# Performance work log

Measured on AMD Instinct MI355X. Metric: run time of the kernel, lower is better.

Reference implementation:

```python
import jax, jax.numpy as jnp
import numpy as np

N_NODES = 20000
N_EDGES = 320000
N_GRAPHS = 256
F_IN = 128
HID = 512


def _xavier(key, shape, gain=1.0):
    fan_out, fan_in = shape
    a = gain * np.sqrt(6.0 / (fan_in + fan_out))
    return jax.random.uniform(key, shape, jnp.float32, -a, a)


def setup_inputs() -> dict:
    key = jax.random.key(0)
    ks = jax.random.split(key, 9)
    x = jax.random.normal(ks[0], (N_NODES, F_IN), jnp.float32)
    edge_index = jax.random.randint(ks[1], (2, N_EDGES), 0, N_NODES, dtype=jnp.int64)
    batch = jnp.sort(jax.random.randint(ks[2], (N_NODES,), 0, N_GRAPHS, dtype=jnp.int64))
    return {
        "x": x,
        "edge_index": edge_index,
        "batch": batch,
        "lin_W": _xavier(ks[3], (HID, F_IN)),
        "lin_b": jnp.zeros((HID,), jnp.float32),
        "W1": _xavier(ks[4], (HID, F_IN)),
        "b1": jnp.zeros((HID,), jnp.float32),
        "W2": _xavier(ks[5], (HID, HID)),
        "b2": jnp.zeros((HID,), jnp.float32),
        "W3": _xavier(ks[6], (HID, HID)),
        "b3": jnp.zeros((HID,), jnp.float32),
        "W4": _xavier(ks[7], (HID, HID)),
        "b4": jnp.zeros((HID,), jnp.float32),
    }


def _gcn_conv(x, W, b, src, dst, norm, n_nodes):
    # PyG GCNConv: h = x @ W.T; out_i = sum_j norm_ij * h_j (scatter over dst) + b
    h = x @ W.T
    msg = h[src] * norm[:, None]  # [E', H] gather + scale
    return jax.ops.segment_sum(msg, dst, num_segments=n_nodes) + b


def reference(x, edge_index, batch, lin_W, lin_b, W1, b1, W2, b2, W3, b3, W4, b4):
    n = x.shape[0]
    loop = jnp.arange(n, dtype=edge_index.dtype)
    src = jnp.concatenate([edge_index[0], loop])
    dst = jnp.concatenate([edge_index[1], loop])
    # symmetric normalization D^-1/2 (A+I) D^-1/2, degree = in-degree over dst
    deg = jax.ops.segment_sum(jnp.ones_like(src, dtype=x.dtype), dst, num_segments=n)
    dis = jnp.where(deg > 0, jax.lax.rsqrt(deg), 0.0)
    norm = dis[src] * dis[dst]

    x_l = x @ lin_W.T + lin_b  # dead code when act=None (kept for faithfulness)

    h1 = _gcn_conv(x, W1, b1, src, dst, norm, n)
    h2 = _gcn_conv(h1, W2, b2, src, dst, norm, n)
    h3 = _gcn_conv(h2, W3, b3, src, dst, norm, n)
    h4 = _gcn_conv(h3, W4, b4, src, dst, norm, n)
    h = jnp.concatenate([h1, h2, h3, h4], axis=1)  # [N, 4*HID]

    h_pooled = jax.ops.segment_max(h, batch, num_segments=N_GRAPHS)
    h_pos = (h > 0).astype(h.dtype)
    counts = jax.ops.segment_sum(jnp.ones((n,), h.dtype), batch, num_segments=N_GRAPHS)
    h_pos_pooled = jax.ops.segment_sum(h_pos, batch, num_segments=N_GRAPHS) / jnp.maximum(counts, 1.0)[:, None]
    return jnp.concatenate([h_pooled, h_pos_pooled], axis=1)  # [G, 8*HID]
```

## Files before the change

### kernel.cpp

```cpp
#include <hip/hip_runtime.h>
#include <cfloat>
#include <cmath>

#define F_IN 128
#define HID 512

typedef short bf16x8 __attribute__((ext_vector_type(8)));
typedef float f32x4 __attribute__((ext_vector_type(4)));

__device__ static inline void split_bf16(float v, short& hi, short& lo) {
    unsigned u = __float_as_uint(v);
    unsigned r = u + 0x7FFF + ((u >> 16) & 1);
    hi = (short)(r >> 16);
    float hf = __uint_as_float(((unsigned)(unsigned short)hi) << 16);
    float res = v - hf;
    unsigned u2 = __float_as_uint(res);
    unsigned r2 = u2 + 0x7FFF + ((u2 >> 16) & 1);
    lo = (short)(r2 >> 16);
}

__device__ static inline void gload_lds16(const void* g, void* l) {
    __builtin_amdgcn_global_load_lds(
        (const __attribute__((address_space(1))) unsigned int*)g,
        (__attribute__((address_space(3))) unsigned int*)l,
        16, 0, 0);
}


__global__ void zero_kernel(int* __restrict__ a, int n) {
    int i = blockIdx.x * blockDim.x + threadIdx.x;
    if (i < n) a[i] = 0;
}

__global__ void count_in_kernel(const int* __restrict__ dst, int* __restrict__ cnt, int E) {
    int e = blockIdx.x * blockDim.x + threadIdx.x;
    if (e < E) atomicAdd(&cnt[dst[e]], 1);
}

__global__ void scan_kernel(const int* __restrict__ cnt, int* __restrict__ offs, int n) {
    __shared__ int buf[1024];
    __shared__ int carry_s;
    if (threadIdx.x == 0) carry_s = 0;
    __syncthreads();
    for (int base = 0; base < n; base += 1024) {
        int i = base + threadIdx.x;
        int v = (i < n) ? cnt[i] : 0;
        buf[threadIdx.x] = v;
        __syncthreads();
        for (int s = 1; s < 1024; s <<= 1) {
            int t = (threadIdx.x >= s) ? buf[threadIdx.x - s] : 0;
            __syncthreads();
            buf[threadIdx.x] += t;
            __syncthreads();
        }
        int total = buf[1023];
        if (i < n) offs[i] = carry_s + buf[threadIdx.x] - v;
        __syncthreads();
        if (threadIdx.x == 0) carry_s += total;
        __syncthreads();
    }
    if (threadIdx.x == 0) offs[n] = carry_s;
}

__global__ void dis_kernel(const int* __restrict__ offs, float* __restrict__ dis, int n) {
    int i = blockIdx.x * blockDim.x + threadIdx.x;
    if (i < n) dis[i] = rsqrtf((float)(offs[i + 1] - offs[i] + 1));
}

__global__ void fill_csr_kernel(const int* __restrict__ src, const int* __restrict__ dst,
                                const int* __restrict__ offs, int* __restrict__ cnt,
                                unsigned short* __restrict__ csr, int E) {
    int e = blockIdx.x * blockDim.x + threadIdx.x;
    if (e < E) {
        int d = dst[e];
        int p = atomicSub(&cnt[d], 1);
        csr[offs[d] + p - 1] = (unsigned short)src[e];
    }
}

__global__ void starts_kernel(const int* __restrict__ batch, int* __restrict__ starts,
                              int n, int G) {
    int i = blockIdx.x * blockDim.x + threadIdx.x;
    if (i >= n) return;
    int b = batch[i];
    if (i == 0) {
        for (int g = 0; g <= b; g++) starts[g] = 0;
    } else {
        int bp = batch[i - 1];
        for (int g = bp + 1; g <= b; g++) starts[g] = i;
    }
    if (i == n - 1) {
        for (int g = b + 1; g <= G; g++) starts[g] = n;
    }
}

__global__ void wconv_kernel(const float* __restrict__ W1, const float* __restrict__ W2,
                             const float* __restrict__ W3, const float* __restrict__ W4,
                             short* __restrict__ Whi, short* __restrict__ Wlo) {
    int i = blockIdx.x * blockDim.x + threadIdx.x;
    const int n1 = HID * F_IN, nk = HID * HID;
    float v;
    if (i < n1) v = W1[i];
    else if (i < n1 + nk) v = W2[i - n1];
    else if (i < n1 + 2 * nk) v = W3[i - n1 - nk];
    else if (i < n1 + 3 * nk) v = W4[i - n1 - 2 * nk];
    else return;
    short h, l;
    split_bf16(v, h, l);
    Whi[i] = h;
    Wlo[i] = l;
}

template <int F, int CHUNKS>
__global__ __launch_bounds__(64) void agg_chunk_kernel(
    const float* __restrict__ H, const float* __restrict__ dis,
    const int* __restrict__ offs, const unsigned short* __restrict__ csr,
    short* __restrict__ Ahi, short* __restrict__ Alo, int n) {
    int blk = blockIdx.x;
    int i = blk / CHUNKS;
    int chunk = blk % CHUNKS;
    int col = chunk * 64 + threadIdx.x;
    const float* Hc = H + col;

    float di = dis[i];
    float a = di * Hc[(size_t)i * F];
    int e = offs[i], e1 = offs[i + 1];
    for (; e + 8 <= e1; e += 8) {
        int j0 = csr[e],     j1 = csr[e + 1], j2 = csr[e + 2], j3 = csr[e + 3];
        int j4 = csr[e + 4], j5 = csr[e + 5], j6 = csr[e + 6], j7 = csr[e + 7];
        float d0 = dis[j0], d1 = dis[j1], d2 = dis[j2], d3 = dis[j3];
        float d4 = dis[j4], d5 = dis[j5], d6 = dis[j6], d7 = dis[j7];
        float r0 = Hc[(size_t)j0 * F], r1 = Hc[(size_t)j1 * F];
        float r2 = Hc[(size_t)j2 * F], r3 = Hc[(size_t)j3 * F];
        float r4 = Hc[(size_t)j4 * F], r5 = Hc[(size_t)j5 * F];
        float r6 = Hc[(size_t)j6 * F], r7 = Hc[(size_t)j7 * F];
        a += d0 * r0 + d1 * r1 + d2 * r2 + d3 * r3;
        a += d4 * r4 + d5 * r5 + d6 * r6 + d7 * r7;
    }
    for (; e < e1; e++) {
        int j = csr[e];
        a += dis[j] * Hc[(size_t)j * F];
    }
    a *= di;
    short h, l;
    split_bf16(a, h, l);
    Ahi[(size_t)i * F + col] = h;
    Alo[(size_t)i * F + col] = l;
}

__global__ __launch_bounds__(256) void gemm_mfma_kernel(
    const short* __restrict__ Ahi, const short* __restrict__ Alo,
    const short* __restrict__ Whi, const short* __restrict__ Wlo,
    const float* __restrict__ bias, float* __restrict__ C,
    int M, int K, int Nout) {
    __shared__ __attribute__((aligned(16))) short lds[4][4096];

    int tid = threadIdx.x;
    int w = tid >> 6, l = tid & 63;
    int m0 = blockIdx.x * 128, n0 = blockIdx.y * 128;
    int lrow = l & 15, lq = l >> 4;

    const short* gp = (w == 0) ? Ahi : (w == 1) ? Alo : (w == 2) ? Whi : Wlo;
    int base_mn = (w < 2) ? m0 : n0;

    f32x4 acc[4][4];
    #pragma unroll
    for (int i = 0; i < 4; i++)
        #pragma unroll
        for (int j = 0; j < 4; j++) acc[i][j] = (f32x4){0.f, 0.f, 0.f, 0.f};

    int wm = w >> 1, wn = w & 1;

    for (int k0 = 0; k0 < K; k0 += 32) {
        const short* gbase = gp + (size_t)(base_mn + lrow) * K + (k0 + lq * 8);
        #pragma unroll
        for (int s = 0; s < 8; s++) {
            gload_lds16(gbase + (size_t)s * 16 * K, &lds[w][s * 64 * 8]);
        }
        __syncthreads();

        bf16x8 ah[4], al[4], wh[4], wl[4];
        #pragma unroll
        for (int i = 0; i < 4; i++) {
            int sA = wm * 4 + i;
            ah[i] = *(const bf16x8*)&lds[0][(sA * 64 + l) * 8];
            al[i] = *(const bf16x8*)&lds[1][(sA * 64 + l) * 8];
            int sW = wn * 4 + i;
            wh[i] = *(const bf16x8*)&lds[2][(sW * 64 + l) * 8];
            wl[i] = *(const bf16x8*)&lds[3][(sW * 64 + l) * 8];
        }
        #pragma unroll
        for (int i = 0; i < 4; i++)
            #pragma unroll
            for (int j = 0; j < 4; j++) {
                acc[i][j] = __builtin_amdgcn_mfma_f32_16x16x32_bf16(ah[i], wh[j], acc[i][j], 0, 0, 0);
                acc[i][j] = __builtin_amdgcn_mfma_f32_16x16x32_bf16(ah[i], wl[j], acc[i][j], 0, 0, 0);
                acc[i][j] = __builtin_amdgcn_mfma_f32_16x16x32_bf16(al[i], wh[j], acc[i][j], 0, 0, 0);
            }
        __syncthreads();
    }

    #pragma unroll
    for (int j = 0; j < 4; j++) {
        int col = n0 + (wn * 4 + j) * 16 + lrow;
        float bv = bias[col];
        #pragma unroll
        for (int i = 0; i < 4; i++) {
            int mrow = m0 + (wm * 4 + i) * 16 + lq * 4;
            #pragma unroll
            for (int r = 0; r < 4; r++) {
                int mm = mrow + r;
                if (mm < M) C[(size_t)mm * Nout + col] = acc[i][j][r] + bv;
            }
        }
    }
}

__global__ void pool_kernel(const float* __restrict__ H, const int* __restrict__ starts,
                            float* __restrict__ out, int layer) {
    int g = blockIdx.x;
    int c = blockIdx.y * 256 + threadIdx.x;
    int s = starts[g], e = starts[g + 1];
    float mx = -INFINITY;
    int pos = 0;
    #pragma unroll 4
    for (int n = s; n < e; n++) {
        float v = H[(size_t)n * HID + c];
        mx = fmaxf(mx, v);
        pos += (v > 0.0f) ? 1 : 0;
    }
    float cntf = fmaxf((float)(e - s), 1.0f);
    out[(size_t)g * (8 * HID) + layer * HID + c] = mx;
    out[(size_t)g * (8 * HID) + 4 * HID + layer * HID + c] = (float)pos / cntf;
}

extern "C" void kernel_launch(void* const* d_in, const int* in_sizes, int n_in,
                              void* d_out, int out_size, void* d_ws, size_t ws_size,
                              hipStream_t stream) {
    const float* x     = (const float*)d_in[0];
    const int*   eidx  = (const int*)d_in[1];
    const int*   batch = (const int*)d_in[2];
    const float* W1 = (const float*)d_in[5];
    const float* b1 = (const float*)d_in[6];
    const float* W2 = (const float*)d_in[7];
    const float* b2 = (const float*)d_in[8];
    const float* W3 = (const float*)d_in[9];
    const float* b3 = (const float*)d_in[10];
    const float* W4 = (const float*)d_in[11];
    const float* b4 = (const float*)d_in[12];
    float* out = (float*)d_out;

    const int N = in_sizes[0] / F_IN;
    const int E = in_sizes[1] / 2;
    const int G = out_size / (8 * HID);

    const int* src = eidx;
    const int* dst = eidx + E;

    const size_t nW = (size_t)HID * F_IN + 3 * (size_t)HID * HID;
    char* w = (char*)d_ws;
    short* Ahi = (short*)w; w += (size_t)N * HID * sizeof(short);
    short* Alo = (short*)w; w += (size_t)N * HID * sizeof(short);
    float* H   = (float*)w; w += (size_t)N * HID * sizeof(float);
    short* Whi = (short*)w; w += nW * sizeof(short);
    short* Wlo = (short*)w; w += nW * sizeof(short);
    int* offs  = (int*)w;   w += (size_t)(N + 4) * sizeof(int);
    unsigned short* csr = (unsigned short*)w; w += (size_t)E * sizeof(unsigned short);
    int* cnt   = (int*)w;   w += (size_t)N * sizeof(int);
    float* dis = (float*)w; w += (size_t)N * sizeof(float);
    int* starts = (int*)w;  w += (size_t)(G + 1) * sizeof(int);

    const size_t wo1 = 0;
    const size_t wo2 = (size_t)HID * F_IN;
    const size_t wo3 = wo2 + (size_t)HID * HID;
    const size_t wo4 = wo3 + (size_t)HID * HID;

    const int TB = 256;
    zero_kernel<<<(N + TB - 1) / TB, TB, 0, stream>>>(cnt, N);
    count_in_kernel<<<(E + TB - 1) / TB, TB, 0, stream>>>(dst, cnt, E);
    scan_kernel<<<1, 1024, 0, stream>>>(cnt, offs, N);
    dis_kernel<<<(N + TB - 1) / TB, TB, 0, stream>>>(offs, dis, N);
    fill_csr_kernel<<<(E + TB - 1) / TB, TB, 0, stream>>>(src, dst, offs, cnt, csr, E);
    starts_kernel<<<(N + TB - 1) / TB, TB, 0, stream>>>(batch, starts, N, G);
    wconv_kernel<<<((int)nW + TB - 1) / TB, TB, 0, stream>>>(W1, W2, W3, W4, Whi, Wlo);

    dim3 gemm_grid((N + 127) / 128, HID / 128);
    dim3 pool_grid(G, HID / 256);

    agg_chunk_kernel<F_IN, 2><<<N * 2, 64, 0, stream>>>(x, dis, offs, csr, Ahi, Alo, N);
    gemm_mfma_kernel<<<gemm_grid, 256, 0, stream>>>(Ahi, Alo, Whi + wo1, Wlo + wo1, b1, H, N, F_IN, HID);
    pool_kernel<<<pool_grid, 256, 0, stream>>>(H, starts, out, 0);

    const size_t wos[3] = {wo2, wo3, wo4};
    const float* bs_[3] = {b2, b3, b4};
    for (int ll = 0; ll < 3; ll++) {
        agg_chunk_kernel<HID, 8><<<N * 8, 64, 0, stream>>>(H, dis, offs, csr, Ahi, Alo, N);
        gemm_mfma_kernel<<<gemm_grid, 256, 0, stream>>>(Ahi, Alo, Whi + wos[ll], Wlo + wos[ll], bs_[ll], H, N, HID, HID);
        pool_kernel<<<pool_grid, 256, 0, stream>>>(H, starts, out, ll + 1);
    }
}
```

Before: 686.2 us.

## Fuse graph pooling into GEMM epilogue via atomics, widen aggregation blocks

Removes the four separate pool kernels by doing segment max and positive-count reduction inside the GEMM epilogue. It uses order-preserving uint encoding with atomicMax and atomicAdd into the output buffer, then runs a final decode/normalise kernel. It also skips writing H for the last layer and merges the dis and starts kernels. The aggregation kernel now handles two nodes per 128-thread block with a 16-wide unrolled gather loop. The cost is more global atomics in the epilogue and extra registers in the GEMM.

```diff
diff --git a/kernel.cpp b/kernel.cpp
--- a/kernel.cpp
+++ b/kernel.cpp
@@ -19,6 +19,11 @@
     lo = (short)(r2 >> 16);
 }
 
+__device__ static inline unsigned enc_f32(float f) {
+    unsigned u = __float_as_uint(f);
+    return (u >> 31) ? ~u : (u | 0x80000000u);
+}
+
 __device__ static inline void gload_lds16(const void* g, void* l) {
     __builtin_amdgcn_global_load_lds(
         (const __attribute__((address_space(1))) unsigned int*)g,
@@ -62,9 +67,22 @@
     if (threadIdx.x == 0) offs[n] = carry_s;
 }
 
-__global__ void dis_kernel(const int* __restrict__ offs, float* __restrict__ dis, int n) {
+__global__ void dis_starts_kernel(const int* __restrict__ offs, float* __restrict__ dis,
+                                  const int* __restrict__ batch, int* __restrict__ starts,
+                                  int n, int G) {
     int i = blockIdx.x * blockDim.x + threadIdx.x;
-    if (i < n) dis[i] = rsqrtf((float)(offs[i + 1] - offs[i] + 1));
+    if (i >= n) return;
+    dis[i] = rsqrtf((float)(offs[i + 1] - offs[i] + 1));
+    int b = batch[i];
+    if (i == 0) {
+        for (int g = 0; g <= b; g++) starts[g] = 0;
+    } else {
+        int bp = batch[i - 1];
+        for (int g = bp + 1; g <= b; g++) starts[g] = i;
+    }
+    if (i == n - 1) {
+        for (int g = b + 1; g <= G; g++) starts[g] = n;
+    }
 }
 
 __global__ void fill_csr_kernel(const int* __restrict__ src, const int* __restrict__ dst,
@@ -75,22 +93,6 @@
         int d = dst[e];
         int p = atomicSub(&cnt[d], 1);
         csr[offs[d] + p - 1] = (unsigned short)src[e];
-    }
-}
-
-__global__ void starts_kernel(const int* __restrict__ batch, int* __restrict__ starts,
-                              int n, int G) {
-    int i = blockIdx.x * blockDim.x + threadIdx.x;
-    if (i >= n) return;
-    int b = batch[i];
-    if (i == 0) {
-        for (int g = 0; g <= b; g++) starts[g] = 0;
-    } else {
-        int bp = batch[i - 1];
-        for (int g = bp + 1; g <= b; g++) starts[g] = i;
-    }
-    if (i == n - 1) {
-        for (int g = b + 1; g <= G; g++) starts[g] = n;
     }
 }
 
@@ -111,31 +113,56 @@
     Wlo[i] = l;
 }
 
+__global__ void pool_init_kernel(unsigned* __restrict__ out, int n) {
+    int i = blockIdx.x * blockDim.x + threadIdx.x;
+    if (i < n) out[i] = ((i & 4095) < 2048) ? 0x007FFFFFu : 0u;
+}
+
+__global__ void pool_fin_kernel(float* __restrict__ out, const int* __restrict__ starts, int G) {
+    int idx = blockIdx.x * blockDim.x + threadIdx.x;
+    if (idx >= G * 2048) return;
+    int g = idx >> 11, lc = idx & 2047;
+    unsigned k = ((unsigned*)out)[(size_t)g * 4096 + lc];
+    unsigned u = (k & 0x80000000u) ? (k & 0x7FFFFFFFu) : ~k;
+    out[(size_t)g * 4096 + lc] = __uint_as_float(u);
+    int cnt = ((int*)out)[(size_t)g * 4096 + 2048 + lc];
+    int nc = starts[g + 1] - starts[g];
+    out[(size_t)g * 4096 + 2048 + lc] = (float)cnt / (float)(nc > 0 ? nc : 1);
+}
+
 template <int F, int CHUNKS>
-__global__ __launch_bounds__(64) void agg_chunk_kernel(
+__global__ __launch_bounds__(128) void agg_chunk_kernel(
     const float* __restrict__ H, const float* __restrict__ dis,
     const int* __restrict__ offs, const unsigned short* __restrict__ csr,
     short* __restrict__ Ahi, short* __restrict__ Alo, int n) {
     int blk = blockIdx.x;
-    int i = blk / CHUNKS;
+    int p = blk / CHUNKS;
     int chunk = blk % CHUNKS;
-    int col = chunk * 64 + threadIdx.x;
+    int i = p * 2 + (threadIdx.x >> 6);
+    if (i >= n) return;
+    int t = threadIdx.x & 63;
+    int col = chunk * 64 + t;
     const float* Hc = H + col;
 
     float di = dis[i];
     float a = di * Hc[(size_t)i * F];
     int e = offs[i], e1 = offs[i + 1];
-    for (; e + 8 <= e1; e += 8) {
-        int j0 = csr[e],     j1 = csr[e + 1], j2 = csr[e + 2], j3 = csr[e + 3];
-        int j4 = csr[e + 4], j5 = csr[e + 5], j6 = csr[e + 6], j7 = csr[e + 7];
+    for (; e + 16 <= e1; e += 16) {
+        int j[16];
+        #pragma unroll
+        for (int q = 0; q < 16; q++) j[q] = csr[e + q];
+        float d[16], r[16];
+        #pragma unroll
+        for (int q = 0; q < 16; q++) { d[q] = dis[j[q]]; r[q] = Hc[(size_t)j[q] * F]; }
+        #pragma unroll
+        for (int q = 0; q < 16; q++) a += d[q] * r[q];
+    }
+    for (; e + 4 <= e1; e += 4) {
+        int j0 = csr[e], j1 = csr[e + 1], j2 = csr[e + 2], j3 = csr[e + 3];
         float d0 = dis[j0], d1 = dis[j1], d2 = dis[j2], d3 = dis[j3];
-        float d4 = dis[j4], d5 = dis[j5], d6 = dis[j6], d7 = dis[j7];
         float r0 = Hc[(size_t)j0 * F], r1 = Hc[(size_t)j1 * F];
         float r2 = Hc[(size_t)j2 * F], r3 = Hc[(size_t)j3 * F];
-        float r4 = Hc[(size_t)j4 * F], r5 = Hc[(size_t)j5 * F];
-        float r6 = Hc[(size_t)j6 * F], r7 = Hc[(size_t)j7 * F];
         a += d0 * r0 + d1 * r1 + d2 * r2 + d3 * r3;
-        a += d4 * r4 + d5 * r5 + d6 * r6 + d7 * r7;
     }
     for (; e < e1; e++) {
         int j = csr[e];
@@ -152,6 +179,7 @@
     const short* __restrict__ Ahi, const short* __restrict__ Alo,
     const short* __restrict__ Whi, const short* __restrict__ Wlo,
     const float* __restrict__ bias, float* __restrict__ C,
+    const int* __restrict__ batch, float* __restrict__ pool, int layer, int write_c,
     int M, int K, int Nout) {
     __shared__ __attribute__((aligned(16))) short lds[4][4096];
 
@@ -200,38 +228,57 @@
         __syncthreads();
     }
 
+    int gcol[4];
+    float bv[4];
     #pragma unroll
     for (int j = 0; j < 4; j++) {
-        int col = n0 + (wn * 4 + j) * 16 + lrow;
-        float bv = bias[col];
-        #pragma unroll
-        for (int i = 0; i < 4; i++) {
-            int mrow = m0 + (wm * 4 + i) * 16 + lq * 4;
-            #pragma unroll
-            for (int r = 0; r < 4; r++) {
-                int mm = mrow + r;
-                if (mm < M) C[(size_t)mm * Nout + col] = acc[i][j][r] + bv;
+        gcol[j] = n0 + (wn * 4 + j) * 16 + lrow;
+        bv[j] = bias[gcol[j]];
+    }
+
+    int curg = -1;
+    float cmax[4];
+    int ccnt[4];
+    #pragma unroll
+    for (int j = 0; j < 4; j++) { cmax[j] = -INFINITY; ccnt[j] = 0; }
+
+    #pragma unroll
+    for (int i = 0; i < 4; i++) {
+        #pragma unroll
+        for (int r = 0; r < 4; r++) {
+            int mm = m0 + (wm * 4 + i) * 16 + lq * 4 + r;
+            if (mm < M) {
+                int g = batch[mm];
+                if (g != curg) {
+                    if (curg >= 0) {
+                        #pragma unroll
+                        for (int j = 0; j < 4; j++) {
+                            size_t base = (size_t)curg * 4096 + layer * HID + gcol[j];
+                            atomicMax((unsigned*)pool + base, enc_f32(cmax[j]));
+                            atomicAdd((int*)pool + base + 2048, ccnt[j]);
+                            cmax[j] = -INFINITY; ccnt[j] = 0;
+                        }
+                    }
+                    curg = g;
+                }
+                #pragma unroll
+                for (int j = 0; j < 4; j++) {
+                    float v = acc[i][j][r] + bv[j];
+                    if (write_c) C[(size_t)mm * Nout + gcol[j]] = v;
+                    cmax[j] = fmaxf(cmax[j], v);
+                    ccnt[j] += (v > 0.0f) ? 1 : 0;
+                }
             }
         }
     }
-}
-
-__global__ void pool_kernel(const float* __restrict__ H, const int* __restrict__ starts,
-                            float* __restrict__ out, int layer) {
-    int g = blockIdx.x;
-    int c = blockIdx.y * 256 + threadIdx.x;
-    int s = starts[g], e = starts[g + 1];
-    float mx = -INFINITY;
-    int pos = 0;
-    #pragma unroll 4
-    for (int n = s; n < e; n++) {
-        float v = H[(size_t)n * HID + c];
-        mx = fmaxf(mx, v);
-        pos += (v > 0.0f) ? 1 : 0;
-    }
-    float cntf = fmaxf((float)(e - s), 1.0f);
-    out[(size_t)g * (8 * HID) + layer * HID + c] = mx;
-    out[(size_t)g * (8 * HID) + 4 * HID + layer * HID + c] = (float)pos / cntf;
+    if (curg >= 0) {
+        #pragma unroll
+        for (int j = 0; j < 4; j++) {
+            size_t base = (size_t)curg * 4096 + layer * HID + gcol[j];
+            atomicMax((unsigned*)pool + base, enc_f32(cmax[j]));
+            atomicAdd((int*)pool + base + 2048, ccnt[j]);
+        }
+    }
 }
 
 extern "C" void kernel_launch(void* const* d_in, const int* in_sizes, int n_in,
@@ -276,26 +323,27 @@
     const size_t wo4 = wo3 + (size_t)HID * HID;
 
     const int TB = 256;
+    pool_init_kernel<<<(G * 4096 + TB - 1) / TB, TB, 0, stream>>>((unsigned*)out, G * 4096);
     zero_kernel<<<(N + TB - 1) / TB, TB, 0, stream>>>(cnt, N);
     count_in_kernel<<<(E + TB - 1) / TB, TB, 0, stream>>>(dst, cnt, E);
     scan_kernel<<<1, 1024, 0, stream>>>(cnt, offs, N);
-    dis_kernel<<<(N + TB - 1) / TB, TB, 0, stream>>>(offs, dis, N);
+    dis_starts_kernel<<<(N + TB - 1) / TB, TB, 0, stream>>>(offs, dis, batch, starts, N, G);
     fill_csr_kernel<<<(E + TB - 1) / TB, TB, 0, stream>>>(src, dst, offs, cnt, csr, E);
-    starts_kernel<<<(N + TB - 1) / TB, TB, 0, stream>>>(batch, starts, N, G);
     wconv_kernel<<<((int)nW + TB - 1) / TB, TB, 0, stream>>>(W1, W2, W3, W4, Whi, Wlo);
 
     dim3 gemm_grid((N + 127) / 128, HID / 128);
-    dim3 pool_grid(G, HID / 256);
-
-    agg_chunk_kernel<F_IN, 2><<<N * 2, 64, 0, stream>>>(x, dis, offs, csr, Ahi, Alo, N);
-    gemm_mfma_kernel<<<gemm_grid, 256, 0, stream>>>(Ahi, Alo, Whi + wo1, Wlo + wo1, b1, H, N, F_IN, HID);
-    pool_kernel<<<pool_grid, 256, 0, stream>>>(H, starts, out, 0);
+
+    agg_chunk_kernel<F_IN, 2><<<((N + 1) / 2) * 2, 128, 0, stream>>>(x, dis, offs, csr, Ahi, Alo, N);
+    gemm_mfma_kernel<<<gemm_grid, 256, 0, stream>>>(Ahi, Alo, Whi + wo1, Wlo + wo1, b1, H,
+                                                    batch, out, 0, 1, N, F_IN, HID);
 
     const size_t wos[3] = {wo2, wo3, wo4};
     const float* bs_[3] = {b2, b3, b4};
     for (int ll = 0; ll < 3; ll++) {
-        agg_chunk_kernel<HID, 8><<<N * 8, 64, 0, stream>>>(H, dis, offs, csr, Ahi, Alo, N);
-        gemm_mfma_kernel<<<gemm_grid, 256, 0, stream>>>(Ahi, Alo, Whi + wos[ll], Wlo + wos[ll], bs_[ll], H, N, HID, HID);
-        pool_kernel<<<pool_grid, 256, 0, stream>>>(H, starts, out, ll + 1);
-    }
-}
+        agg_chunk_kernel<HID, 8><<<((N + 1) / 2) * 8, 128, 0, stream>>>(H, dis, offs, csr, Ahi, Alo, N);
+        gemm_mfma_kernel<<<gemm_grid, 256, 0, stream>>>(Ahi, Alo, Whi + wos[ll], Wlo + wos[ll], bs_[ll], H,
+                                                        batch, out, ll + 1, (ll < 2) ? 1 : 0, N, HID, HID);
+    }
+
+    pool_fin_kernel<<<(G * 2048 + TB - 1) / TB, TB, 0, stream>>>(out, starts, G);
+}
```

Result: slower. 726.9 us (+5.9%).
